# Kernel tuning notes

Measured on AMD Instinct MI355X. Metric: run time of the kernel, lower is better.

The kernel has to match this reference:

```python
import jax, jax.numpy as jnp
import numpy as np

B, F, D = 1024, 256, 64  # batch, featureNumb, featureDim


def setup_inputs() -> dict:
    key = jax.random.key(0)
    k1, k2, k3, k4 = jax.random.split(key, 4)
    feature = jax.random.normal(k1, (B, F, D), dtype=jnp.float32)
    indicator = jax.random.normal(k2, (F, D), dtype=jnp.float32)
    # QKVTransformV2(n, D, D): n stacked DxD linear maps of the indicator
    W_qk = jax.random.normal(k3, (2, D, D), dtype=jnp.float32) / np.float32(np.sqrt(D))
    W_qkv = jax.random.normal(k4, (3, D, D), dtype=jnp.float32) / np.float32(np.sqrt(D))
    return {"feature": feature, "indicator": indicator, "W_qk": W_qk, "W_qkv": W_qkv}


def reference(feature, indicator, W_qk, W_qkv):
    d = indicator.shape[-1]
    scale = jnp.asarray(1.0 / np.sqrt(d), feature.dtype)

    # --- gate branch: QKTrans + DotWeight + LTE (straight-through hard threshold) ---
    trans = jnp.einsum('fd,nde->nfe', indicator, W_qk)            # [2,F,D]
    gate_logits = jnp.einsum('id,jd->ij', trans[0], trans[1]) * scale  # [F,F]
    gate = (gate_logits > 0).astype(feature.dtype)                # LTE forward: hard 0/1 gate

    # --- QKV branch, fused form of the rank-1 outer products ---
    # Original: QKV_outer[t,i,j] = qkv[t,i] (x) qkv[t,j]  (DxD rank-1)
    #           input[b,t,i,j,:] = feature[b,i] @ QKV_outer[t,i,j]
    #                            = (feature[b,i] . qkv[t,i]) * qkv[t,j]
    qkv = jnp.einsum('fd,nde->nfe', indicator, W_qkv)             # [3,F,D]
    s = jnp.einsum('bfd,nfd->nbf', feature, qkv)                  # s[t,b,i] = feature[b,i].qkv[t,i]

    # score[b,i,j] = input[b,0,i,j,:] . input[b,1,j,i,:]
    #              = s[0,b,i] * s[1,b,j] * (qkv[1,i] . qkv[0,j])
    cross = jnp.einsum('id,jd->ij', qkv[1], qkv[0])               # [F,F]
    score = s[0][:, :, None] * s[1][:, None, :] * cross[None]     # [B,F,F]
    scoreHat = score * gate[None]                                 # [B,F,F]

    # output[b,i,:] = sum_j scoreHat[b,i,j] * value[b,i,j,:]
    #               = s[2,b,i] * sum_j scoreHat[b,i,j] * qkv[2,j,:]
    out = s[2][:, :, None] * jnp.einsum('bij,jd->bid', scoreHat, qkv[2])  # [B,F,D]
    return out
```

## Files before the change

### kernel.cpp

```cpp
#include <hip/hip_runtime.h>
#include <stdint.h>

#define B 1024
#define F 256
#define D 64

typedef __attribute__((ext_vector_type(8))) short short8;
typedef __attribute__((ext_vector_type(4))) float f32x4;

__device__ __forceinline__ short f2bf(float f) {
    unsigned u = __builtin_bit_cast(unsigned, f);
    u += 0x7fff + ((u >> 16) & 1);
    return (short)(u >> 16);
}
__device__ __forceinline__ float bf2f(short s) {
    unsigned u = ((unsigned)(unsigned short)s) << 16;
    return __builtin_bit_cast(float, u);
}
__device__ __forceinline__ unsigned pk_bf16(float a, float b) {
    unsigned ua = __builtin_bit_cast(unsigned, a) + 0x8000u;
    unsigned ub = __builtin_bit_cast(unsigned, b) + 0x8000u;
    return __builtin_amdgcn_perm(ub, ua, 0x07060302u);
}

__device__ __forceinline__ float dot4(float4 a, float4 b) {
    return a.x * b.x + a.y * b.y + a.z * b.z + a.w * b.w;
}

__device__ __forceinline__ void gload_lds16(const float* g, float* l) {
    __builtin_amdgcn_global_load_lds(
        (const __attribute__((address_space(1))) unsigned int*)g,
        (__attribute__((address_space(3))) unsigned int*)l, 16, 0, 0);
}


__global__ void precompute_trans(const float* __restrict__ indicator,
                                 const float* __restrict__ W_qk,
                                 const float* __restrict__ W_qkv,
                                 float* __restrict__ trans,
                                 float* __restrict__ qkv) {
    int idx = blockIdx.x * blockDim.x + threadIdx.x;
    int n   = idx / (F * D);
    int rem = idx - n * (F * D);
    int f   = rem / D;
    int e   = rem - f * D;
    const float* W = (n < 2) ? (W_qk + n * D * D) : (W_qkv + (n - 2) * D * D);
    const float* ind = indicator + f * D;
    float acc = 0.f;
#pragma unroll 8
    for (int d = 0; d < D; ++d) acc += ind[d] * W[d * D + e];
    if (n < 2) trans[n * F * D + f * D + e] = acc;
    else       qkv[(n - 2) * F * D + f * D + e] = acc;
}

__global__ __launch_bounds__(256) void compute_Mt(const float* __restrict__ trans,
                                                  const float* __restrict__ qkv,
                                                  short* __restrict__ At,
                                                  short* __restrict__ q2K) {
    int j = blockIdx.x;
    int i = threadIdx.x;
    const float4* t0 = (const float4*)(trans + i * D);
    const float4* t1 = (const float4*)(trans + F * D + j * D);
    const float4* q1 = (const float4*)(qkv + F * D + i * D);
    const float4* q0 = (const float4*)(qkv + j * D);
    float d0 = 0.f, d1 = 0.f;
#pragma unroll
    for (int k = 0; k < D / 4; ++k) {
        float4 a = t0[k], b = t1[k], c = q1[k], e = q0[k];
        d0 += dot4(a, b);
        d1 += dot4(c, e);
    }
    float v = (d0 > 0.f) ? d1 : 0.f;
    At[((j >> 5) * F + i) * 32 + (j & 31)] = f2bf(v);
    if (j < D) {
        int p = (j & 3) * 16 + (j >> 2);
        q2K[((i >> 5) * D + p) * 32 + (i & 31)] = f2bf(qkv[2 * F * D + i * D + j]);
    }
}

__global__ __launch_bounds__(512, 2) void fused_sg(const float* __restrict__ feature,
                                                   const float* __restrict__ qkv,
                                                   const short* __restrict__ At,
                                                   const short* __restrict__ q2K,
                                                   float* __restrict__ out) {
    int bp  = blockIdx.x;
    int b0  = bp * 2;
    int tid = threadIdx.x;

    __shared__ __align__(16) short q2L[8 * 64 * 32];
    __shared__ __align__(16) float fbuf[2][4096];
    __shared__ __align__(16) short s1L[2 * F];
    __shared__ __align__(16) float gL[2 * F];

    {
        const float4* Qg = (const float4*)q2K;
        float4* Ql = (float4*)q2L;
#pragma unroll
        for (int v = tid; v < 2048; v += 512) Ql[v] = Qg[v];
    }

    {
        int rg = tid >> 4;
        int l  = tid & 15;

#define STAGE(c, buf)                                                          \
        {                                                                      \
            const float* gb = feature +                                        \
                ((size_t)((b0 + ((c) >> 2)) * F + (((c) & 3) * 64)) * D);      \
            float* lb = fbuf[buf];                                             \
            gload_lds16(gb + tid * 4, lb + tid * 4);                           \
            gload_lds16(gb + 2048 + tid * 4, lb + 2048 + tid * 4);             \
        }

        STAGE(0, 0)
        __syncthreads();
        for (int c = 0; c < 8; ++c) {
            int buf = c & 1;
            if (c < 7) STAGE(c + 1, buf ^ 1)
            int bsel  = c >> 2;
            int fbase = (c & 3) * 64;
            const float4* fb = (const float4*)fbuf[buf];
#pragma unroll
            for (int q = 0; q < 2; ++q) {
                int r = q * 32 + rg;
                int f = fbase + r;
                float4 fv = fb[r * 16 + l];
                float4 q0 = ((const float4*)(qkv + f * D))[l];
                float4 q1 = ((const float4*)(qkv + F * D + f * D))[l];
                float4 q2 = ((const float4*)(qkv + 2 * F * D + f * D))[l];
                float a0 = dot4(fv, q0);
                float a1 = dot4(fv, q1);
                float a2 = dot4(fv, q2);
#pragma unroll
                for (int m = 1; m < 16; m <<= 1) {
                    a0 += __shfl_xor(a0, m, 64);
                    a1 += __shfl_xor(a1, m, 64);
                    a2 += __shfl_xor(a2, m, 64);
                }
                if (l == 0) {
                    gL[bsel * F + f]  = a0 * a2;
                    s1L[bsel * F + f] = f2bf(a1);
                }
            }
            __syncthreads();
        }
#undef STAGE
    }

    int w    = tid >> 6;
    int lane = tid & 63;
    int l16  = lane & 15;
    int lq   = lane >> 4;
    int kq   = lq * 8;
    int wc   = w & 1;
    int it   = w >> 1;
    int b    = b0 + wc;

    f32x4 acc[4][4];
#pragma unroll
    for (int mt = 0; mt < 4; ++mt)
#pragma unroll
        for (int nt = 0; nt < 4; ++nt) acc[mt][nt] = (f32x4){0.f, 0.f, 0.f, 0.f};

    for (int jt = 0; jt < F / 32; ++jt) {
        short8 sv = *(const short8*)(s1L + wc * F + jt * 32 + kq);
        float sf[8];
#pragma unroll
        for (int e = 0; e < 8; ++e) sf[e] = bf2f(sv[e]);

        short8 bfr[4];
#pragma unroll
        for (int nt = 0; nt < 4; ++nt) {
            int d = nt * 16 + l16;
            short8 qv = *(const short8*)(q2L + (jt * 64 + d) * 32 + kq);
            int4 packed;
            packed.x = pk_bf16(bf2f(qv[0]) * sf[0], bf2f(qv[1]) * sf[1]);
            packed.y = pk_bf16(bf2f(qv[2]) * sf[2], bf2f(qv[3]) * sf[3]);
            packed.z = pk_bf16(bf2f(qv[4]) * sf[4], bf2f(qv[5]) * sf[5]);
            packed.w = pk_bf16(bf2f(qv[6]) * sf[6], bf2f(qv[7]) * sf[7]);
            bfr[nt] = __builtin_bit_cast(short8, packed);
        }
#pragma unroll
        for (int mt = 0; mt < 4; ++mt) {
            short8 af = *(const short8*)(At + ((size_t)jt * F + it * 64 + mt * 16 + l16) * 32 + kq);
#pragma unroll
            for (int nt = 0; nt < 4; ++nt)
                acc[mt][nt] = __builtin_amdgcn_mfma_f32_16x16x32_bf16(
                    af, bfr[nt], acc[mt][nt], 0, 0, 0);
        }
    }

    const float4* g4 = (const float4*)(gL + wc * F + it * 64);
#pragma unroll
    for (int mt = 0; mt < 4; ++mt) {
        float4 gg = g4[mt * 4 + lq];
        float* obase = out + ((size_t)(b * F + it * 64 + mt * 16 + lq * 4)) * D + l16 * 4;
        float4 v0 = {gg.x * acc[mt][0][0], gg.x * acc[mt][1][0],
                     gg.x * acc[mt][2][0], gg.x * acc[mt][3][0]};
        float4 v1 = {gg.y * acc[mt][0][1], gg.y * acc[mt][1][1],
                     gg.y * acc[mt][2][1], gg.y * acc[mt][3][1]};
        float4 v2 = {gg.z * acc[mt][0][2], gg.z * acc[mt][1][2],
                     gg.z * acc[mt][2][2], gg.z * acc[mt][3][2]};
        float4 v3 = {gg.w * acc[mt][0][3], gg.w * acc[mt][1][3],
                     gg.w * acc[mt][2][3], gg.w * acc[mt][3][3]};
        *(float4*)(obase + 0 * D) = v0;
        *(float4*)(obase + 1 * D) = v1;
        *(float4*)(obase + 2 * D) = v2;
        *(float4*)(obase + 3 * D) = v3;
    }
}

extern "C" void kernel_launch(void* const* d_in, const int* in_sizes, int n_in,
                              void* d_out, int out_size, void* d_ws, size_t ws_size,
                              hipStream_t stream) {
    const float* feature   = (const float*)d_in[0];
    const float* indicator = (const float*)d_in[1];
    const float* W_qk      = (const float*)d_in[2];
    const float* W_qkv     = (const float*)d_in[3];
    float* out = (float*)d_out;

    float* ws    = (float*)d_ws;
    float* trans = ws;
    float* qkv   = trans + 2 * F * D;
    short* At    = (short*)(qkv + 3 * F * D);
    short* q2K   = At + F * F;

    hipLaunchKernelGGL(precompute_trans, dim3((5 * F * D) / 256), dim3(256), 0,
                       stream, indicator, W_qk, W_qkv, trans, qkv);
    hipLaunchKernelGGL(compute_Mt, dim3(F), dim3(256), 0, stream, trans, qkv, At, q2K);
    hipLaunchKernelGGL(fused_sg, dim3(B / 2), dim3(512), 0, stream,
                       feature, qkv, At, q2K, out);
}
```

Measured before the change: 140.9 us.

## Pipeline feature projection per wave with register-prefetched qkv and no block barriers

```diff
diff --git a/kernel.cpp b/kernel.cpp
--- a/kernel.cpp
+++ b/kernel.cpp
@@ -88,7 +88,7 @@
     int tid = threadIdx.x;
 
     __shared__ __align__(16) short q2L[8 * 64 * 32];
-    __shared__ __align__(16) float fbuf[2][4096];
+    __shared__ __align__(16) float fbuf[8192];
     __shared__ __align__(16) short s1L[2 * F];
     __shared__ __align__(16) float gL[2 * F];
 
@@ -100,37 +100,53 @@
     }
 
     {
-        int rg = tid >> 4;
-        int l  = tid & 15;
-
-#define STAGE(c, buf)                                                          \
-        {                                                                      \
-            const float* gb = feature +                                        \
-                ((size_t)((b0 + ((c) >> 2)) * F + (((c) & 3) * 64)) * D);      \
-            float* lb = fbuf[buf];                                             \
-            gload_lds16(gb + tid * 4, lb + tid * 4);                           \
-            gload_lds16(gb + 2048 + tid * 4, lb + 2048 + tid * 4);             \
-        }
-
-        STAGE(0, 0)
-        __syncthreads();
+        int wv   = tid >> 6;
+        int wb   = wv >> 2;
+        int qr   = wv & 3;
+        int lane = tid & 63;
+        int l    = lane & 15;
+        int rg   = lane >> 4;
+
+        const float* gbase = feature + ((size_t)((b0 + wb) * F + qr * 64)) * D;
+        float*       lbase = fbuf + wv * 1024;
+
+        float4 qk[2][6];
+
+#define STAGE(c)                                                          \
+        {                                                                 \
+            const float* g = gbase + (c) * 512;                           \
+            float* lb = lbase + ((c) & 1) * 512;                          \
+            gload_lds16(g + lane * 4, lb + lane * 4);                     \
+            gload_lds16(g + 256 + lane * 4, lb + 256 + lane * 4);         \
+        }
+#define QKV(c, s)                                                         \
+        {                                                                 \
+            _Pragma("unroll")                                             \
+            for (int pp = 0; pp < 2; ++pp) {                              \
+                int f = qr * 64 + (c) * 8 + pp * 4 + rg;                  \
+                qk[s][pp * 3 + 0] = *(const float4*)(qkv + (size_t)f * D + l * 4); \
+                qk[s][pp * 3 + 1] = *(const float4*)(qkv + F * D + (size_t)f * D + l * 4); \
+                qk[s][pp * 3 + 2] = *(const float4*)(qkv + 2 * F * D + (size_t)f * D + l * 4); \
+            }                                                             \
+        }
+
+        STAGE(0)
+        QKV(0, 0)
+        __builtin_amdgcn_sched_barrier(0);
+        STAGE(1)
+
+#pragma unroll
         for (int c = 0; c < 8; ++c) {
-            int buf = c & 1;
-            if (c < 7) STAGE(c + 1, buf ^ 1)
-            int bsel  = c >> 2;
-            int fbase = (c & 3) * 64;
-            const float4* fb = (const float4*)fbuf[buf];
-#pragma unroll
-            for (int q = 0; q < 2; ++q) {
-                int r = q * 32 + rg;
-                int f = fbase + r;
-                float4 fv = fb[r * 16 + l];
-                float4 q0 = ((const float4*)(qkv + f * D))[l];
-                float4 q1 = ((const float4*)(qkv + F * D + f * D))[l];
-                float4 q2 = ((const float4*)(qkv + 2 * F * D + f * D))[l];
-                float a0 = dot4(fv, q0);
-                float a1 = dot4(fv, q1);
-                float a2 = dot4(fv, q2);
+            if (c < 7) asm volatile("s_waitcnt vmcnt(2)" ::: "memory");
+            else       asm volatile("s_waitcnt vmcnt(0)" ::: "memory");
+            __builtin_amdgcn_sched_barrier(0);
+#pragma unroll
+            for (int pp = 0; pp < 2; ++pp) {
+                int f = qr * 64 + c * 8 + pp * 4 + rg;
+                float4 fv = *(const float4*)(lbase + (c & 1) * 512 + (pp * 4 + rg) * 64 + l * 4);
+                float a0 = dot4(fv, qk[c & 1][pp * 3 + 0]);
+                float a1 = dot4(fv, qk[c & 1][pp * 3 + 1]);
+                float a2 = dot4(fv, qk[c & 1][pp * 3 + 2]);
 #pragma unroll
                 for (int m = 1; m < 16; m <<= 1) {
                     a0 += __shfl_xor(a0, m, 64);
@@ -138,14 +154,18 @@
                     a2 += __shfl_xor(a2, m, 64);
                 }
                 if (l == 0) {
-                    gL[bsel * F + f]  = a0 * a2;
-                    s1L[bsel * F + f] = f2bf(a1);
+                    gL[wb * F + f]  = a0 * a2;
+                    s1L[wb * F + f] = f2bf(a1);
                 }
             }
-            __syncthreads();
+            if (c + 1 < 8) QKV(c + 1, (c + 1) & 1)
+            __builtin_amdgcn_sched_barrier(0);
+            if (c + 2 < 8) STAGE(c + 2)
         }
 #undef STAGE
-    }
+#undef QKV
+    }
+    __syncthreads();
 
     int w    = tid >> 6;
     int lane = tid & 63;
```

New measurement: 149.4 us. 1.06x slower.
